# Performance work log

Measured on AMD Instinct MI355X. Metric: run time of the kernel, lower is better.

The kernel has to match this reference:

```python
import jax, jax.numpy as jnp
import numpy as np

E = 384      # n_embed
H = 6        # n_head
HS = E // H  # head_size = 64
B = 64
T = 256      # == block_size
FF = 4 * E


def _layernorm(x, g, b, eps=1e-5):
    m = x.mean(-1, keepdims=True)
    v = ((x - m) ** 2).mean(-1, keepdims=True)
    return (x - m) / jnp.sqrt(v + eps) * g + b


def _mha(q_in, k_in, v_in, wq, bq, wk, bk, wv, bv, pw, pb):
    # Faithful to source: scale uses q_in's last dim (n_embed=384), NOT head_size,
    # and the causal tril mask is applied even in cross-attention.
    scale = q_in.shape[-1] ** -0.5
    q = jnp.einsum('bte,hes->bhts', q_in, wq) + bq[None, :, None, :]  # [B,H,T1,HS]
    k = jnp.einsum('bue,hes->bhus', k_in, wk) + bk[None, :, None, :]  # [B,H,T2,HS]
    v = jnp.einsum('bue,hes->bhus', v_in, wv) + bv[None, :, None, :]
    wei = jnp.einsum('bhts,bhus->bhtu', q, k) * scale                 # [B,H,T1,T2]
    T1, T2 = q_in.shape[1], k_in.shape[1]
    mask = jnp.tril(jnp.ones((T1, T2), dtype=bool))
    wei = jnp.where(mask[None, None], wei, -jnp.inf)
    wei = jax.nn.softmax(wei, axis=-1)
    out = jnp.einsum('bhtu,bhus->bths', wei, v)                       # [B,T1,H,HS]
    out = out.reshape(out.shape[0], out.shape[1], -1)                 # concat heads
    return out @ pw + pb


def setup_inputs() -> dict:
    key = jax.random.key(0)
    ks = jax.random.split(key, 32)
    s = 0.02
    d = {
        'encode_output': jax.random.normal(ks[0], (B, T, E), jnp.float32),
        'x': jax.random.normal(ks[1], (B, T, E), jnp.float32),
    }
    i = 2
    for p in ('sa1', 'sa2'):
        d[p + '_wq'] = jax.random.normal(ks[i], (H, E, HS), jnp.float32) * s; i += 1
        d[p + '_bq'] = jnp.zeros((H, HS), jnp.float32)
        d[p + '_wk'] = jax.random.normal(ks[i], (H, E, HS), jnp.float32) * s; i += 1
        d[p + '_bk'] = jnp.zeros((H, HS), jnp.float32)
        d[p + '_wv'] = jax.random.normal(ks[i], (H, E, HS), jnp.float32) * s; i += 1
        d[p + '_bv'] = jnp.zeros((H, HS), jnp.float32)
        d[p + '_pw'] = jax.random.normal(ks[i], (E, E), jnp.float32) * s; i += 1
        d[p + '_pb'] = jnp.zeros((E,), jnp.float32)
    d['ff_w1'] = jax.random.normal(ks[i], (E, FF), jnp.float32) * s; i += 1
    d['ff_b1'] = jnp.zeros((FF,), jnp.float32)
    d['ff_w2'] = jax.random.normal(ks[i], (FF, E), jnp.float32) * s; i += 1
    d['ff_b2'] = jnp.zeros((E,), jnp.float32)
    for n in ('ln1', 'ln2', 'ln3'):
        d[n + '_g'] = jnp.ones((E,), jnp.float32)
        d[n + '_b'] = jnp.zeros((E,), jnp.float32)
    return d


def reference(encode_output, x,
              sa1_wq, sa1_bq, sa1_wk, sa1_bk, sa1_wv, sa1_bv, sa1_pw, sa1_pb,
              sa2_wq, sa2_bq, sa2_wk, sa2_bk, sa2_wv, sa2_bv, sa2_pw, sa2_pb,
              ff_w1, ff_b1, ff_w2, ff_b2,
              ln1_g, ln1_b, ln2_g, ln2_b, ln3_g, ln3_b):
    # masked self-attention + add&norm
    a1 = _mha(x, x, x, sa1_wq, sa1_bq, sa1_wk, sa1_bk, sa1_wv, sa1_bv, sa1_pw, sa1_pb)
    o1 = _layernorm(x + a1, ln1_g, ln1_b)
    # cross-attention (q=o1, k=v=encode_output) + add&norm
    a2 = _mha(o1, encode_output, encode_output,
              sa2_wq, sa2_bq, sa2_wk, sa2_bk, sa2_wv, sa2_bv, sa2_pw, sa2_pb)
    o2 = _layernorm(o1 + a2, ln2_g, ln2_b)
    # FFN + add&norm
    f = jax.nn.relu(o2 @ ff_w1 + ff_b1) @ ff_w2 + ff_b2
    return _layernorm(o2 + f, ln3_g, ln3_b)
```

## Files before the change

### kernel.cpp

```cpp
#include <hip/hip_runtime.h>

typedef __attribute__((ext_vector_type(8))) short bf16x8;
typedef __attribute__((ext_vector_type(4))) float f32x4;

__device__ __forceinline__ float b2f(ushort b) {
    union { unsigned int u; float f; } x;
    x.u = ((unsigned int)b) << 16;
    return x.f;
}
__device__ __forceinline__ ushort f2b(float f) {
    union { float f; unsigned int u; } x;
    x.f = f;
    unsigned int r = x.u + 0x7fffu + ((x.u >> 16) & 1u);
    return (ushort)(r >> 16);
}
__device__ __forceinline__ int4 pack8(float4 a, float4 b) {
    union { int4 v; ushort u[8]; } r;
    r.u[0] = f2b(a.x); r.u[1] = f2b(a.y); r.u[2] = f2b(a.z); r.u[3] = f2b(a.w);
    r.u[4] = f2b(b.x); r.u[5] = f2b(b.y); r.u[6] = f2b(b.z); r.u[7] = f2b(b.w);
    return r.v;
}
__device__ __forceinline__ int4 add_resb(int4 cs, int4 rs) {
    const ushort* c = (const ushort*)&cs; const ushort* r = (const ushort*)&rs;
    union { int4 v; ushort u[8]; } o;
#pragma unroll
    for (int j = 0; j < 8; j++) o.u[j] = f2b(b2f(c[j]) + b2f(r[j]));
    return o.v;
}
__device__ __forceinline__ int4 add_resf(int4 cs, float4 r0, float4 r1) {
    const ushort* c = (const ushort*)&cs;
    const float* rf0 = (const float*)&r0; const float* rf1 = (const float*)&r1;
    union { int4 v; ushort u[8]; } o;
#pragma unroll
    for (int j = 0; j < 4; j++) o.u[j] = f2b(b2f(c[j]) + rf0[j]);
#pragma unroll
    for (int j = 0; j < 4; j++) o.u[4 + j] = f2b(b2f(c[4 + j]) + rf1[j]);
    return o.v;
}

__device__ __forceinline__ void gll16(const ushort* g, ushort* l) {
    __builtin_amdgcn_global_load_lds(
        (__attribute__((address_space(1))) void*)(g),
        (__attribute__((address_space(3))) void*)(l), 16, 0, 0);
}

template<int MI>
__global__ __launch_bounds__(256) void gemm_bs(
    const ushort* __restrict__ A, const ushort* __restrict__ Bt,
    ushort* __restrict__ C, const float* __restrict__ bias,
    const ushort* __restrict__ resb, const float* __restrict__ resf,
    int N, int K, int relu)
{
    __shared__ __align__(16) ushort sm[24576];
    constexpr int CHUNK = MI * 64;
    constexpr int PERX  = (16384 / CHUNK) / 8;
    const int tid  = threadIdx.x;
    const int wave = tid >> 6, lane = tid & 63;
    const int qd = lane >> 4, lc = lane & 15;
    const int id = blockIdx.x, xcd = id & 7, sub = id >> 3;
    const int mc = sub % PERX, ct = sub / PERX;
    const int row0 = (xcd * PERX + mc) * CHUNK;
    const int col0 = ct * 64;

    f32x4 acc[MI][4];
#pragma unroll
    for (int i = 0; i < MI; i++)
#pragma unroll
        for (int j = 0; j < 4; j++) acc[i][j] = 0.0f;

    const ushort* Aw = A + (size_t)(row0 + wave * MI * 16 + lc) * K + qd * 8;
    const ushort* Bw = Bt + (size_t)(col0 + wave * 16 + (lane >> 2)) * K + (lane & 3) * 8;
    ushort* Bsw = &sm[wave * 512];

    const int NKC = K / 384;
    for (int kc = 0; kc < NKC; ++kc) {
        if (kc) __syncthreads();
#pragma unroll
        for (int j = 0; j < 12; j++)
            gll16(Bw + kc * 384 + j * 32, Bsw + j * 2048);
        __syncthreads();

        const ushort* Akc = Aw + kc * 384;
#pragma unroll
        for (int kk = 0; kk < 12; ++kk) {
            bf16x8 af[MI];
#pragma unroll
            for (int mi = 0; mi < MI; mi++)
                af[mi] = *(const bf16x8*)(Akc + (size_t)mi * 16 * K + kk * 32);
            bf16x8 bfr[4];
#pragma unroll
            for (int ni = 0; ni < 4; ni++)
                bfr[ni] = *(const bf16x8*)&sm[kk * 2048 + (ni * 16 + lc) * 32 + qd * 8];
            __builtin_amdgcn_s_setprio(1);
#pragma unroll
            for (int mi = 0; mi < MI; mi++)
#pragma unroll
                for (int ni = 0; ni < 4; ni++)
                    acc[mi][ni] = __builtin_amdgcn_mfma_f32_16x16x32_bf16(
                        af[mi], bfr[ni], acc[mi][ni], 0, 0, 0);
            __builtin_amdgcn_s_setprio(0);
        }
    }

    __syncthreads();
    ushort* Csw = &sm[wave * MI * 16 * 68];
#pragma unroll
    for (int mi = 0; mi < MI; mi++)
#pragma unroll
        for (int r = 0; r < 4; r++) {
            int lr = mi * 16 + qd * 4 + r;
#pragma unroll
            for (int ni = 0; ni < 4; ni++) {
                float v = acc[mi][ni][r];
                if (bias) v += bias[col0 + ni * 16 + lc];
                if (relu) v = fmaxf(v, 0.0f);
                Csw[lr * 68 + ni * 16 + lc] = f2b(v);
            }
        }
    asm volatile("s_waitcnt lgkmcnt(0)" ::: "memory");
    const int rowW = row0 + wave * MI * 16;
#pragma unroll
    for (int p = 0; p < MI * 2; p++) {
        int lr = p * 8 + (lane >> 3), cc = (lane & 7) * 8;
        size_t base = (size_t)(rowW + lr) * N + col0 + cc;
        int4 d = *(const int4*)&Csw[lr * 68 + cc];
        if (resb) d = add_resb(d, *(const int4*)&resb[base]);
        else if (resf) d = add_resf(d, *(const float4*)&resf[base],
                                       *(const float4*)&resf[base + 4]);
        *(int4*)&C[base] = d;
    }
}

__global__ __launch_bounds__(256) void gemm_bs_dual(
    const ushort* __restrict__ A1, const ushort* __restrict__ B1t,
    ushort* __restrict__ C1, const float* __restrict__ bias1, int N1,
    const ushort* __restrict__ A2, const ushort* __restrict__ B2t,
    ushort* __restrict__ C2, const float* __restrict__ bias2, int N2,
    int split)
{
    __shared__ __align__(16) ushort sm[24576];
    const int K = 384;
    const int tid  = threadIdx.x;
    const int wave = tid >> 6, lane = tid & 63;
    const int qd = lane >> 4, lc = lane & 15;
    const int id = blockIdx.x, xcd = id & 7, sub = id >> 3;
    const int mc = sub & 15, ct = sub >> 4;
    const int row0 = (xcd * 16 + mc) * 128;
    const bool first = ct < split;
    const ushort* A  = first ? A1 : A2;
    const ushort* Bt = first ? B1t : B2t;
    ushort* C        = first ? C1 : C2;
    const float* bias = first ? bias1 : bias2;
    const int N      = first ? N1 : N2;
    const int col0   = (first ? ct : ct - split) * 64;

    f32x4 acc[2][4];
#pragma unroll
    for (int i = 0; i < 2; i++)
#pragma unroll
        for (int j = 0; j < 4; j++) acc[i][j] = 0.0f;

    const ushort* Aw = A + (size_t)(row0 + wave * 32 + lc) * K + qd * 8;
    const ushort* Bw = Bt + (size_t)(col0 + wave * 16 + (lane >> 2)) * K + (lane & 3) * 8;
    ushort* Bsw = &sm[wave * 512];

#pragma unroll
    for (int j = 0; j < 12; j++)
        gll16(Bw + j * 32, Bsw + j * 2048);
    __syncthreads();

#pragma unroll
    for (int kk = 0; kk < 12; ++kk) {
        bf16x8 af[2];
#pragma unroll
        for (int mi = 0; mi < 2; mi++)
            af[mi] = *(const bf16x8*)(Aw + (size_t)mi * 16 * K + kk * 32);
        bf16x8 bfr[4];
#pragma unroll
        for (int ni = 0; ni < 4; ni++)
            bfr[ni] = *(const bf16x8*)&sm[kk * 2048 + (ni * 16 + lc) * 32 + qd * 8];
        __builtin_amdgcn_s_setprio(1);
#pragma unroll
        for (int mi = 0; mi < 2; mi++)
#pragma unroll
            for (int ni = 0; ni < 4; ni++)
                acc[mi][ni] = __builtin_amdgcn_mfma_f32_16x16x32_bf16(
                    af[mi], bfr[ni], acc[mi][ni], 0, 0, 0);
        __builtin_amdgcn_s_setprio(0);
    }

    __syncthreads();
    ushort* Csw = &sm[wave * 32 * 68];
#pragma unroll
    for (int mi = 0; mi < 2; mi++)
#pragma unroll
        for (int r = 0; r < 4; r++) {
            int lr = mi * 16 + qd * 4 + r;
#pragma unroll
            for (int ni = 0; ni < 4; ni++)
                Csw[lr * 68 + ni * 16 + lc] = f2b(acc[mi][ni][r] + bias[col0 + ni * 16 + lc]);
        }
    asm volatile("s_waitcnt lgkmcnt(0)" ::: "memory");
    const int rowW = row0 + wave * 32;
#pragma unroll
    for (int p = 0; p < 4; p++) {
        int lr = p * 8 + (lane >> 3), cc = (lane & 7) * 8;
        size_t base = (size_t)(rowW + lr) * N + col0 + cc;
        *(int4*)&C[base] = *(const int4*)&Csw[lr * 68 + cc];
    }
}

__global__ __launch_bounds__(256) void attn(
    const ushort* __restrict__ q, int qstr,
    const ushort* __restrict__ k, int kstr,
    const ushort* __restrict__ v, int vstr,
    ushort* __restrict__ out)
{
    __shared__ __align__(16) ushort Qs[64 * 72];
    __shared__ __align__(16) ushort Kc[64 * 72];
    __shared__ __align__(16) ushort Vc[64 * 72];
    __shared__ __align__(16) ushort Ps[64 * 264];

    const int tid = threadIdx.x;
    const int wave = tid >> 6, lane = tid & 63;
    const int qd = lane >> 4, lc = lane & 15;
    const int b = blockIdx.z, h = blockIdx.y, t0 = blockIdx.x * 64;
    const int hc = h * 64;
    const float scale = 0.051031036307982884f;

    {
        int r = tid >> 2, c = (tid & 3) * 16;
        int4 q0 = *(const int4*)&q[(size_t)(b * 256 + t0 + r) * qstr + hc + c];
        int4 q1 = *(const int4*)&q[(size_t)(b * 256 + t0 + r) * qstr + hc + c + 8];
        *(int4*)&Qs[r * 72 + c] = q0;
        *(int4*)&Qs[r * 72 + c + 8] = q1;
    }

    f32x4 accS[16];
#pragma unroll
    for (int j = 0; j < 16; j++) accS[j] = 0.0f;

    for (int uc = 0; uc < 4; uc++) {
        int r = tid >> 2, c = (tid & 3) * 16;
        int4 k0v = *(const int4*)&k[(size_t)(b * 256 + uc * 64 + r) * kstr + hc + c];
        int4 k1v = *(const int4*)&k[(size_t)(b * 256 + uc * 64 + r) * kstr + hc + c + 8];
        __syncthreads();
        *(int4*)&Kc[r * 72 + c] = k0v;
        *(int4*)&Kc[r * 72 + c + 8] = k1v;
        __syncthreads();
#pragma unroll
        for (int s0 = 0; s0 < 64; s0 += 32) {
            bf16x8 a = *(const bf16x8*)&Qs[(wave * 16 + lc) * 72 + s0 + qd * 8];
#pragma unroll
            for (int ni = 0; ni < 4; ni++) {
                bf16x8 bb = *(const bf16x8*)&Kc[(ni * 16 + lc) * 72 + s0 + qd * 8];
                accS[uc * 4 + ni] =
                    __builtin_amdgcn_mfma_f32_16x16x32_bf16(a, bb, accS[uc * 4 + ni], 0, 0, 0);
            }
        }
    }

#pragma unroll
    for (int rr = 0; rr < 4; rr++) {
        int t = t0 + wave * 16 + qd * 4 + rr;
        float pv[16];
        float mx = -3.0e38f;
#pragma unroll
        for (int j = 0; j < 16; j++) {
            int u = (j >> 2) * 64 + (j & 3) * 16 + lc;
            float s = accS[j][rr] * scale;
            s = (u <= t) ? s : -3.0e38f;
            pv[j] = s;
            mx = fmaxf(mx, s);
        }
#pragma unroll
        for (int m = 1; m < 16; m <<= 1) mx = fmaxf(mx, __shfl_xor(mx, m, 16));
        float sum = 0.0f;
#pragma unroll
        for (int j = 0; j < 16; j++) { float p = __expf(pv[j] - mx); pv[j] = p; sum += p; }
#pragma unroll
        for (int m = 1; m < 16; m <<= 1) sum += __shfl_xor(sum, m, 16);
        float inv = 1.0f / sum;
#pragma unroll
        for (int j = 0; j < 16; j++) {
            int u = (j >> 2) * 64 + (j & 3) * 16 + lc;
            Ps[(wave * 16 + qd * 4 + rr) * 264 + u] = f2b(pv[j] * inv);
        }
    }

    f32x4 accO[4];
#pragma unroll
    for (int j = 0; j < 4; j++) accO[j] = 0.0f;
    for (int uc = 0; uc < 4; uc++) {
        int r = tid >> 2, s0 = (tid & 3) * 16;
        int4 v0 = *(const int4*)&v[(size_t)(b * 256 + uc * 64 + r) * vstr + hc + s0];
        int4 v1 = *(const int4*)&v[(size_t)(b * 256 + uc * 64 + r) * vstr + hc + s0 + 8];
        __syncthreads();
        {
            const ushort* t0p = (const ushort*)&v0;
            const ushort* t1p = (const ushort*)&v1;
#pragma unroll
            for (int j = 0; j < 8; j++) Vc[(s0 + j) * 72 + r] = t0p[j];
#pragma unroll
            for (int j = 0; j < 8; j++) Vc[(s0 + 8 + j) * 72 + r] = t1p[j];
        }
        __syncthreads();
#pragma unroll
        for (int u0 = 0; u0 < 64; u0 += 32) {
            bf16x8 a = *(const bf16x8*)&Ps[(wave * 16 + lc) * 264 + uc * 64 + u0 + qd * 8];
#pragma unroll
            for (int ni = 0; ni < 4; ni++) {
                bf16x8 bb = *(const bf16x8*)&Vc[(ni * 16 + lc) * 72 + u0 + qd * 8];
                accO[ni] = __builtin_amdgcn_mfma_f32_16x16x32_bf16(a, bb, accO[ni], 0, 0, 0);
            }
        }
    }

#pragma unroll
    for (int ni = 0; ni < 4; ni++)
#pragma unroll
        for (int rr = 0; rr < 4; rr++) {
            int t = t0 + wave * 16 + qd * 4 + rr;
            out[(size_t)(b * 256 + t) * 384 + hc + ni * 16 + lc] = f2b(accO[ni][rr]);
        }
}

__global__ __launch_bounds__(256) void lnorm(
    const ushort* __restrict__ in, const float* __restrict__ g,
    const float* __restrict__ be, ushort* __restrict__ outb,
    float* __restrict__ outf)
{
    const int wave = threadIdx.x >> 6, lane = threadIdx.x & 63;
    const int row = blockIdx.x * 4 + wave;
    const ushort* r = in + (size_t)row * 384;
    float x[6], s1 = 0.0f, s2 = 0.0f;
#pragma unroll
    for (int j = 0; j < 6; j++) {
        x[j] = b2f(r[j * 64 + lane]);
        s1 += x[j]; s2 += x[j] * x[j];
    }
#pragma unroll
    for (int m = 1; m < 64; m <<= 1) {
        s1 += __shfl_xor(s1, m, 64);
        s2 += __shfl_xor(s2, m, 64);
    }
    float mean = s1 * (1.0f / 384.0f);
    float var  = s2 * (1.0f / 384.0f) - mean * mean;
    float rstd = rsqrtf(var + 1e-5f);
#pragma unroll
    for (int j = 0; j < 6; j++) {
        float y = (x[j] - mean) * rstd * g[j * 64 + lane] + be[j * 64 + lane];
        if (outb) outb[(size_t)row * 384 + j * 64 + lane] = f2b(y);
        if (outf) outf[(size_t)row * 384 + j * 64 + lane] = y;
    }
}

__device__ __forceinline__ void dev_cvt(const float* in, ushort* out, int blk) {
    size_t i = ((size_t)blk * 256 + threadIdx.x) * 8;
    float4 a = *(const float4*)(in + i);
    float4 b = *(const float4*)(in + i + 4);
    *(int4*)(out + i) = pack8(a, b);
}
__device__ __forceinline__ void dev_transp(const float* in, ushort* out,
                                           int R, int C, int bx, int by,
                                           float (*t)[33]) {
    const int tx = threadIdx.x & 31, ty = threadIdx.x >> 5;
    const int c0 = bx * 32, r0 = by * 32;
#pragma unroll
    for (int i = 0; i < 32; i += 8)
        t[ty + i][tx] = in[(size_t)(r0 + ty + i) * C + c0 + tx];
    __syncthreads();
#pragma unroll
    for (int i = 0; i < 32; i += 8)
        out[(size_t)(c0 + ty + i) * R + r0 + tx] = f2b(t[tx][ty + i]);
}
__device__ __forceinline__ void dev_packqkv(const float* wq, const float* wk,
                                            const float* wv, ushort* Wt,
                                            int blk, float (*t)[33]) {
    const int tx = threadIdx.x & 31, ty = threadIdx.x >> 5;
    const int bx = blk % 12, by = (blk / 12) % 2, bz = blk / 24;
    const int e0 = bx * 32, s0 = by * 32;
    const int seg = bz / 6, h = bz - seg * 6;
    const float* w = (seg == 0) ? wq : (seg == 1) ? wk : wv;
    const float* wh = w + (size_t)h * 384 * 64;
#pragma unroll
    for (int i = 0; i < 32; i += 8)
        t[ty + i][tx] = wh[(size_t)(e0 + ty + i) * 64 + s0 + tx];
    __syncthreads();
    const int nbase = seg * 384 + h * 64 + s0;
#pragma unroll
    for (int i = 0; i < 32; i += 8)
        Wt[(size_t)(nbase + ty + i) * 384 + e0 + tx] = f2b(t[tx][ty + i]);
}

__global__ __launch_bounds__(256) void prep_all(
    const float* __restrict__ x, ushort* __restrict__ xb,
    const float* __restrict__ enc, ushort* __restrict__ encb,
    const float* __restrict__ s1wq, const float* __restrict__ s1wk,
    const float* __restrict__ s1wv, ushort* __restrict__ W1,
    const float* __restrict__ s2wq, const float* __restrict__ s2wk,
    const float* __restrict__ s2wv, ushort* __restrict__ W2,
    const float* __restrict__ s1pw, ushort* __restrict__ pw1t,
    const float* __restrict__ s2pw, ushort* __restrict__ pw2t,
    const float* __restrict__ fw1, ushort* __restrict__ w1t,
    const float* __restrict__ fw2, ushort* __restrict__ w2t,
    const float* __restrict__ s1bq, const float* __restrict__ s1bk,
    const float* __restrict__ s1bv, const float* __restrict__ s2bq,
    const float* __restrict__ s2bk, const float* __restrict__ s2bv,
    float* __restrict__ bias1, float* __restrict__ bias2)
{
    __shared__ float t[32][33];
    int blk = blockIdx.x;
    if (blk < 3072) { dev_cvt(x, xb, blk); return; }
    blk -= 3072;
    if (blk < 3072) { dev_cvt(enc, encb, blk); return; }
    blk -= 3072;
    if (blk < 432) { dev_packqkv(s1wq, s1wk, s1wv, W1, blk, t); return; }
    blk -= 432;
    if (blk < 432) { dev_packqkv(s2wq, s2wk, s2wv, W2, blk, t); return; }
    blk -= 432;
    if (blk < 144) { dev_transp(s1pw, pw1t, 384, 384, blk % 12, blk / 12, t); return; }
    blk -= 144;
    if (blk < 144) { dev_transp(s2pw, pw2t, 384, 384, blk % 12, blk / 12, t); return; }
    blk -= 144;
    if (blk < 576) { dev_transp(fw1, w1t, 384, 1536, blk % 48, blk / 48, t); return; }
    blk -= 576;
    if (blk < 576) { dev_transp(fw2, w2t, 1536, 384, blk % 12, blk / 12, t); return; }
    blk -= 576;
    int i = blk * 256 + threadIdx.x;
    if (i >= 2304) return;
    int grp = i / 1152, r = i - grp * 1152;
    int seg = r / 384, nn = r - seg * 384;
    const float* src = grp == 0 ? (seg == 0 ? s1bq : seg == 1 ? s1bk : s1bv)
                                : (seg == 0 ? s2bq : seg == 1 ? s2bk : s2bv);
    (grp == 0 ? bias1 : bias2)[r] = src[nn];
}

extern "C" void kernel_launch(void* const* d_in, const int* in_sizes, int n_in,
                              void* d_out, int out_size, void* d_ws, size_t ws_size,
                              hipStream_t stream)
{
    const float* enc = (const float*)d_in[0];
    const float* x   = (const float*)d_in[1];
    const float* s1wq = (const float*)d_in[2];  const float* s1bq = (const float*)d_in[3];
    const float* s1wk = (const float*)d_in[4];  const float* s1bk = (const float*)d_in[5];
    const float* s1wv = (const float*)d_in[6];  const float* s1bv = (const float*)d_in[7];
    const float* s1pw = (const float*)d_in[8];  const float* s1pb = (const float*)d_in[9];
    const float* s2wq = (const float*)d_in[10]; const float* s2bq = (const float*)d_in[11];
    const float* s2wk = (const float*)d_in[12]; const float* s2bk = (const float*)d_in[13];
    const float* s2wv = (const float*)d_in[14]; const float* s2bv = (const float*)d_in[15];
    const float* s2pw = (const float*)d_in[16]; const float* s2pb = (const float*)d_in[17];
    const float* fw1 = (const float*)d_in[18];  const float* fb1 = (const float*)d_in[19];
    const float* fw2 = (const float*)d_in[20];  const float* fb2 = (const float*)d_in[21];
    const float* g1 = (const float*)d_in[22];   const float* be1 = (const float*)d_in[23];
    const float* g2 = (const float*)d_in[24];   const float* be2 = (const float*)d_in[25];
    const float* g3 = (const float*)d_in[26];   const float* be3 = (const float*)d_in[27];

    if (ws_size < 80216064u) return;

    ushort* wsp = (ushort*)d_ws;
    ushort* qkv1 = wsp;
    ushort* q2   = wsp;
    ushort* kv2  = wsp + 6291456;
    ushort* h1   = wsp;
    ushort* att  = wsp + 18874368;
    ushort* xb   = wsp + 18874368;
    ushort* tmp  = wsp + 25165824;
    ushort* o1b  = wsp + 31457280;
    ushort* W1   = wsp + 37748736;
    ushort* W2   = W1 + 442368;
    ushort* pw1t = W2 + 442368;
    ushort* pw2t = pw1t + 147456;
    ushort* w1t  = pw2t + 147456;
    ushort* w2t  = w1t + 589824;

    ushort* encb = (ushort*)d_out;
    ushort* o2b  = (ushort*)d_out;
    float* bias1 = (float*)((ushort*)d_out + 6291456);
    float* bias2 = bias1 + 1152;

    prep_all<<<dim3(8457), dim3(256), 0, stream>>>(
        x, xb, enc, encb,
        s1wq, s1wk, s1wv, W1, s2wq, s2wk, s2wv, W2,
        s1pw, pw1t, s2pw, pw2t, fw1, w1t, fw2, w2t,
        s1bq, s1bk, s1bv, s2bq, s2bk, s2bv, bias1, bias2);

    gemm_bs<4><<<dim3(1152), dim3(256), 0, stream>>>(
        xb, W1, qkv1, bias1, nullptr, nullptr, 1152, 384, 0);
    attn<<<dim3(4, 6, 64), dim3(256), 0, stream>>>(
        qkv1, 1152, qkv1 + 384, 1152, qkv1 + 768, 1152, att);
    gemm_bs<2><<<dim3(768), dim3(256), 0, stream>>>(
        att, pw1t, tmp, s1pb, nullptr, x, 384, 384, 0);
    lnorm<<<dim3(4096), dim3(256), 0, stream>>>(tmp, g1, be1, o1b, nullptr);

    gemm_bs_dual<<<dim3(2304), dim3(256), 0, stream>>>(
        o1b, W2, q2, bias2, 384,
        encb, W2 + 147456, kv2, bias2 + 384, 768, 6);
    attn<<<dim3(4, 6, 64), dim3(256), 0, stream>>>(
        q2, 384, kv2, 768, kv2 + 384, 768, att);
    gemm_bs<2><<<dim3(768), dim3(256), 0, stream>>>(
        att, pw2t, tmp, s2pb, o1b, nullptr, 384, 384, 0);
    lnorm<<<dim3(4096), dim3(256), 0, stream>>>(tmp, g2, be2, o2b, nullptr);

    gemm_bs<4><<<dim3(1536), dim3(256), 0, stream>>>(
        o2b, w1t, h1, fb1, nullptr, nullptr, 1536, 384, 1);
    gemm_bs<2><<<dim3(768), dim3(256), 0, stream>>>(
        h1, w2t, tmp, fb2, o2b, nullptr, 384, 1536, 0);
    lnorm<<<dim3(4096), dim3(256), 0, stream>>>(tmp, g3, be3, nullptr, (float*)d_out);
}
```

Baseline: 468.5 us.

## Software-pipeline A global loads and double-buffer B LDS fragments in GEMM kernels

Both GEMM kernels now prefetch A fragments from global memory three k-steps ahead into a 4-slot register ring. They also double-buffer the B fragments read from shared memory one k-step ahead. Explicit s_waitcnt with vmcnt/lgkmcnt thresholds plus a sched_barrier are placed before the MFMA block, so memory latency overlaps with matrix math instead of stalling each step. The cost is higher register pressure. The hand-written wait counts are also loose in the tail iterations where no new loads are issued, so correctness there relies on the compiler's own waits.

```diff
diff --git a/kernel.cpp b/kernel.cpp
--- a/kernel.cpp
+++ b/kernel.cpp
@@ -42,6 +42,14 @@
     __builtin_amdgcn_global_load_lds(
         (__attribute__((address_space(1))) void*)(g),
         (__attribute__((address_space(3))) void*)(l), 16, 0, 0);
+}
+
+template<int MI> __device__ __forceinline__ void wait_pipe();
+template<> __device__ __forceinline__ void wait_pipe<4>() {
+    asm volatile("s_waitcnt vmcnt(12) lgkmcnt(4)" ::: "memory");
+}
+template<> __device__ __forceinline__ void wait_pipe<2>() {
+    asm volatile("s_waitcnt vmcnt(6) lgkmcnt(4)" ::: "memory");
 }
 
 template<int MI>
@@ -72,32 +80,50 @@
     const ushort* Bw = Bt + (size_t)(col0 + wave * 16 + (lane >> 2)) * K + (lane & 3) * 8;
     ushort* Bsw = &sm[wave * 512];
 
+    bf16x8 pre[4][MI];
+    bf16x8 bfr[2][4];
+
     const int NKC = K / 384;
     for (int kc = 0; kc < NKC; ++kc) {
         if (kc) __syncthreads();
 #pragma unroll
         for (int j = 0; j < 12; j++)
             gll16(Bw + kc * 384 + j * 32, Bsw + j * 2048);
+        const ushort* Akc = Aw + kc * 384;
+#pragma unroll
+        for (int g = 0; g < 3; g++)
+#pragma unroll
+            for (int mi = 0; mi < MI; mi++)
+                pre[g][mi] = *(const bf16x8*)(Akc + (size_t)mi * 16 * K + g * 32);
         __syncthreads();
 
-        const ushort* Akc = Aw + kc * 384;
+#pragma unroll
+        for (int ni = 0; ni < 4; ni++)
+            bfr[0][ni] = *(const bf16x8*)&sm[(ni * 16 + lc) * 32 + qd * 8];
+
 #pragma unroll
         for (int kk = 0; kk < 12; ++kk) {
-            bf16x8 af[MI];
-#pragma unroll
-            for (int mi = 0; mi < MI; mi++)
-                af[mi] = *(const bf16x8*)(Akc + (size_t)mi * 16 * K + kk * 32);
-            bf16x8 bfr[4];
-#pragma unroll
-            for (int ni = 0; ni < 4; ni++)
-                bfr[ni] = *(const bf16x8*)&sm[kk * 2048 + (ni * 16 + lc) * 32 + qd * 8];
+            if (kk < 9) {
+#pragma unroll
+                for (int mi = 0; mi < MI; mi++)
+                    pre[(kk + 3) & 3][mi] =
+                        *(const bf16x8*)(Akc + (size_t)mi * 16 * K + (kk + 3) * 32);
+            }
+            if (kk < 11) {
+#pragma unroll
+                for (int ni = 0; ni < 4; ni++)
+                    bfr[(kk + 1) & 1][ni] =
+                        *(const bf16x8*)&sm[(kk + 1) * 2048 + (ni * 16 + lc) * 32 + qd * 8];
+            }
+            wait_pipe<MI>();
+            __builtin_amdgcn_sched_barrier(0);
             __builtin_amdgcn_s_setprio(1);
 #pragma unroll
             for (int mi = 0; mi < MI; mi++)
 #pragma unroll
                 for (int ni = 0; ni < 4; ni++)
                     acc[mi][ni] = __builtin_amdgcn_mfma_f32_16x16x32_bf16(
-                        af[mi], bfr[ni], acc[mi][ni], 0, 0, 0);
+                        pre[kk & 3][mi], bfr[kk & 1][ni], acc[mi][ni], 0, 0, 0);
             __builtin_amdgcn_s_setprio(0);
         }
     }
@@ -164,28 +190,46 @@
     const ushort* Bw = Bt + (size_t)(col0 + wave * 16 + (lane >> 2)) * K + (lane & 3) * 8;
     ushort* Bsw = &sm[wave * 512];
 
+    bf16x8 pre[4][2];
+    bf16x8 bfr[2][4];
+
 #pragma unroll
     for (int j = 0; j < 12; j++)
         gll16(Bw + j * 32, Bsw + j * 2048);
+#pragma unroll
+    for (int g = 0; g < 3; g++)
+#pragma unroll
+        for (int mi = 0; mi < 2; mi++)
+            pre[g][mi] = *(const bf16x8*)(Aw + (size_t)mi * 16 * K + g * 32);
     __syncthreads();
 
 #pragma unroll
+    for (int ni = 0; ni < 4; ni++)
+        bfr[0][ni] = *(const bf16x8*)&sm[(ni * 16 + lc) * 32 + qd * 8];
+
+#pragma unroll
     for (int kk = 0; kk < 12; ++kk) {
-        bf16x8 af[2];
-#pragma unroll
-        for (int mi = 0; mi < 2; mi++)
-            af[mi] = *(const bf16x8*)(Aw + (size_t)mi * 16 * K + kk * 32);
-        bf16x8 bfr[4];
-#pragma unroll
-        for (int ni = 0; ni < 4; ni++)
-            bfr[ni] = *(const bf16x8*)&sm[kk * 2048 + (ni * 16 + lc) * 32 + qd * 8];
+        if (kk < 9) {
+#pragma unroll
+            for (int mi = 0; mi < 2; mi++)
+                pre[(kk + 3) & 3][mi] =
+                    *(const bf16x8*)(Aw + (size_t)mi * 16 * K + (kk + 3) * 32);
+        }
+        if (kk < 11) {
+#pragma unroll
+            for (int ni = 0; ni < 4; ni++)
+                bfr[(kk + 1) & 1][ni] =
+                    *(const bf16x8*)&sm[(kk + 1) * 2048 + (ni * 16 + lc) * 32 + qd * 8];
+        }
+        wait_pipe<2>();
+        __builtin_amdgcn_sched_barrier(0);
         __builtin_amdgcn_s_setprio(1);
 #pragma unroll
         for (int mi = 0; mi < 2; mi++)
 #pragma unroll
             for (int ni = 0; ni < 4; ni++)
                 acc[mi][ni] = __builtin_amdgcn_mfma_f32_16x16x32_bf16(
-                    af[mi], bfr[ni], acc[mi][ni], 0, 0, 0);
+                    pre[kk & 3][mi], bfr[kk & 1][ni], acc[mi][ni], 0, 0, 0);
         __builtin_amdgcn_s_setprio(0);
     }
 
```

New measurement: 478.6 us. 2.2% more time.

## Prefetch A fragments into registers and unify GEMMs on 128-row tiles

Applied to the files above, without the earlier changes.

Each K-chunk's A fragments are now loaded into a 12x2 register array before the LDS barrier, so the global loads overlap the B-to-LDS transfer instead of being issued one k-step at a time inside the MFMA loop. The MI=4 template variant is removed and every GEMM uses 128-row tiles, which doubles the grid for the QKV and FFN-up GEMMs. Launch bounds now request 2 blocks per SM. The register prefetch raises VGPR pressure, and the smaller tiles reread B more often.

```diff
diff --git a/kernel.cpp b/kernel.cpp
--- a/kernel.cpp
+++ b/kernel.cpp
@@ -44,31 +44,28 @@
         (__attribute__((address_space(3))) void*)(l), 16, 0, 0);
 }
 
-template<int MI>
-__global__ __launch_bounds__(256) void gemm_bs(
+__global__ __launch_bounds__(256, 2) void gemm_bs(
     const ushort* __restrict__ A, const ushort* __restrict__ Bt,
     ushort* __restrict__ C, const float* __restrict__ bias,
     const ushort* __restrict__ resb, const float* __restrict__ resf,
     int N, int K, int relu)
 {
     __shared__ __align__(16) ushort sm[24576];
-    constexpr int CHUNK = MI * 64;
-    constexpr int PERX  = (16384 / CHUNK) / 8;
     const int tid  = threadIdx.x;
     const int wave = tid >> 6, lane = tid & 63;
     const int qd = lane >> 4, lc = lane & 15;
     const int id = blockIdx.x, xcd = id & 7, sub = id >> 3;
-    const int mc = sub % PERX, ct = sub / PERX;
-    const int row0 = (xcd * PERX + mc) * CHUNK;
+    const int mc = sub & 15, ct = sub >> 4;
+    const int row0 = (xcd * 16 + mc) * 128;
     const int col0 = ct * 64;
 
-    f32x4 acc[MI][4];
-#pragma unroll
-    for (int i = 0; i < MI; i++)
+    f32x4 acc[2][4];
+#pragma unroll
+    for (int i = 0; i < 2; i++)
 #pragma unroll
         for (int j = 0; j < 4; j++) acc[i][j] = 0.0f;
 
-    const ushort* Aw = A + (size_t)(row0 + wave * MI * 16 + lc) * K + qd * 8;
+    const ushort* Aw = A + (size_t)(row0 + wave * 32 + lc) * K + qd * 8;
     const ushort* Bw = Bt + (size_t)(col0 + wave * 16 + (lane >> 2)) * K + (lane & 3) * 8;
     ushort* Bsw = &sm[wave * 512];
 
@@ -78,34 +75,36 @@
 #pragma unroll
         for (int j = 0; j < 12; j++)
             gll16(Bw + kc * 384 + j * 32, Bsw + j * 2048);
+        const ushort* Akc = Aw + kc * 384;
+        bf16x8 a[12][2];
+#pragma unroll
+        for (int kk = 0; kk < 12; kk++)
+#pragma unroll
+            for (int mi = 0; mi < 2; mi++)
+                a[kk][mi] = *(const bf16x8*)(Akc + (size_t)mi * 16 * K + kk * 32);
         __syncthreads();
 
-        const ushort* Akc = Aw + kc * 384;
 #pragma unroll
         for (int kk = 0; kk < 12; ++kk) {
-            bf16x8 af[MI];
-#pragma unroll
-            for (int mi = 0; mi < MI; mi++)
-                af[mi] = *(const bf16x8*)(Akc + (size_t)mi * 16 * K + kk * 32);
             bf16x8 bfr[4];
 #pragma unroll
             for (int ni = 0; ni < 4; ni++)
                 bfr[ni] = *(const bf16x8*)&sm[kk * 2048 + (ni * 16 + lc) * 32 + qd * 8];
             __builtin_amdgcn_s_setprio(1);
 #pragma unroll
-            for (int mi = 0; mi < MI; mi++)
+            for (int mi = 0; mi < 2; mi++)
 #pragma unroll
                 for (int ni = 0; ni < 4; ni++)
                     acc[mi][ni] = __builtin_amdgcn_mfma_f32_16x16x32_bf16(
-                        af[mi], bfr[ni], acc[mi][ni], 0, 0, 0);
+                        a[kk][mi], bfr[ni], acc[mi][ni], 0, 0, 0);
             __builtin_amdgcn_s_setprio(0);
         }
     }
 
     __syncthreads();
-    ushort* Csw = &sm[wave * MI * 16 * 68];
-#pragma unroll
-    for (int mi = 0; mi < MI; mi++)
+    ushort* Csw = &sm[wave * 32 * 68];
+#pragma unroll
+    for (int mi = 0; mi < 2; mi++)
 #pragma unroll
         for (int r = 0; r < 4; r++) {
             int lr = mi * 16 + qd * 4 + r;
@@ -118,9 +117,9 @@
             }
         }
     asm volatile("s_waitcnt lgkmcnt(0)" ::: "memory");
-    const int rowW = row0 + wave * MI * 16;
-#pragma unroll
-    for (int p = 0; p < MI * 2; p++) {
+    const int rowW = row0 + wave * 32;
+#pragma unroll
+    for (int p = 0; p < 4; p++) {
         int lr = p * 8 + (lane >> 3), cc = (lane & 7) * 8;
         size_t base = (size_t)(rowW + lr) * N + col0 + cc;
         int4 d = *(const int4*)&Csw[lr * 68 + cc];
@@ -131,7 +130,7 @@
     }
 }
 
-__global__ __launch_bounds__(256) void gemm_bs_dual(
+__global__ __launch_bounds__(256, 2) void gemm_bs_dual(
     const ushort* __restrict__ A1, const ushort* __restrict__ B1t,
     ushort* __restrict__ C1, const float* __restrict__ bias1, int N1,
     const ushort* __restrict__ A2, const ushort* __restrict__ B2t,
@@ -167,14 +166,16 @@
 #pragma unroll
     for (int j = 0; j < 12; j++)
         gll16(Bw + j * 32, Bsw + j * 2048);
+    bf16x8 a[12][2];
+#pragma unroll
+    for (int kk = 0; kk < 12; kk++)
+#pragma unroll
+        for (int mi = 0; mi < 2; mi++)
+            a[kk][mi] = *(const bf16x8*)(Aw + (size_t)mi * 16 * K + kk * 32);
     __syncthreads();
 
 #pragma unroll
     for (int kk = 0; kk < 12; ++kk) {
-        bf16x8 af[2];
-#pragma unroll
-        for (int mi = 0; mi < 2; mi++)
-            af[mi] = *(const bf16x8*)(Aw + (size_t)mi * 16 * K + kk * 32);
         bf16x8 bfr[4];
 #pragma unroll
         for (int ni = 0; ni < 4; ni++)
@@ -185,7 +186,7 @@
 #pragma unroll
             for (int ni = 0; ni < 4; ni++)
                 acc[mi][ni] = __builtin_amdgcn_mfma_f32_16x16x32_bf16(
-                    af[mi], bfr[ni], acc[mi][ni], 0, 0, 0);
+                    a[kk][mi], bfr[ni], acc[mi][ni], 0, 0, 0);
         __builtin_amdgcn_s_setprio(0);
     }
 
@@ -485,11 +486,11 @@
         s1pw, pw1t, s2pw, pw2t, fw1, w1t, fw2, w2t,
         s1bq, s1bk, s1bv, s2bq, s2bk, s2bv, bias1, bias2);
 
-    gemm_bs<4><<<dim3(1152), dim3(256), 0, stream>>>(
+    gemm_bs<<<dim3(2304), dim3(256), 0, stream>>>(
         xb, W1, qkv1, bias1, nullptr, nullptr, 1152, 384, 0);
     attn<<<dim3(4, 6, 64), dim3(256), 0, stream>>>(
         qkv1, 1152, qkv1 + 384, 1152, qkv1 + 768, 1152, att);
-    gemm_bs<2><<<dim3(768), dim3(256), 0, stream>>>(
+    gemm_bs<<<dim3(768), dim3(256), 0, stream>>>(
         att, pw1t, tmp, s1pb, nullptr, x, 384, 384, 0);
     lnorm<<<dim3(4096), dim3(256), 0, stream>>>(tmp, g1, be1, o1b, nullptr);
 
@@ -498,13 +499,13 @@
         encb, W2 + 147456, kv2, bias2 + 384, 768, 6);
     attn<<<dim3(4, 6, 64), dim3(256), 0, stream>>>(
         q2, 384, kv2, 768, kv2 + 384, 768, att);
-    gemm_bs<2><<<dim3(768), dim3(256), 0, stream>>>(
+    gemm_bs<<<dim3(768), dim3(256), 0, stream>>>(
         att, pw2t, tmp, s2pb, o1b, nullptr, 384, 384, 0);
     lnorm<<<dim3(4096), dim3(256), 0, stream>>>(tmp, g2, be2, o2b, nullptr);
 
-    gemm_bs<4><<<dim3(1536), dim3(256), 0, stream>>>(
+    gemm_bs<<<dim3(3072), dim3(256), 0, stream>>>(
         o2b, w1t, h1, fb1, nullptr, nullptr, 1536, 384, 1);
-    gemm_bs<2><<<dim3(768), dim3(256), 0, stream>>>(
+    gemm_bs<<<dim3(768), dim3(256), 0, stream>>>(
         h1, w2t, tmp, fb2, o2b, nullptr, 384, 1536, 0);
     lnorm<<<dim3(4096), dim3(256), 0, stream>>>(tmp, g3, be3, nullptr, (float*)d_out);
 }
```

Result: slower. 501.9 us (+7.1%).
